# Performance work log

Hardware: AMD Instinct MI355X
Metric: run time of the kernel (lower is better)

The kernel has to match this reference:

```python
import jax, jax.numpy as jnp
import numpy as np

VOCAB = 256
D = 512
L = 2
FFN = 2048
H = 8
HD = D // H  # head dim = random-feature dim m for favor+
B = 2
T = 2048


def setup_inputs() -> dict:
    key = jax.random.key(0)
    ks = jax.random.split(key, 16)
    rng = np.random.default_rng(0)

    def lin(k, fan_in, shape):
        return jax.random.normal(k, shape, jnp.float32) / np.sqrt(fan_in)

    tokens = jax.random.randint(ks[0], (B, T), 0, VOCAB)
    emb = jax.random.normal(ks[1], (VOCAB, D // 2), jnp.float32)
    Wq = lin(ks[2], D, (L, D, D)); bq = 0.01 * jax.random.normal(ks[3], (L, D), jnp.float32)
    Wk = lin(ks[4], D, (L, D, D)); bk = 0.01 * jax.random.normal(ks[5], (L, D), jnp.float32)
    Wv = lin(ks[6], D, (L, D, D)); bv = 0.01 * jax.random.normal(ks[7], (L, D), jnp.float32)
    WU = lin(ks[8], D, (L, D, FFN)); bU = 0.01 * jax.random.normal(ks[9], (L, FFN), jnp.float32)
    WV = lin(ks[10], FFN, (L, FFN, D)); bV = 0.01 * jax.random.normal(ks[11], (L, D), jnp.float32)
    Wout = lin(ks[12], D, (D, VOCAB)); bout = 0.01 * jax.random.normal(ks[13], (VOCAB,), jnp.float32)
    ln1_g = jnp.ones((L, D), jnp.float32) + 0.02 * jax.random.normal(ks[14], (L, D), jnp.float32)
    ln2_g = jnp.ones((L, D), jnp.float32) + 0.02 * jax.random.normal(ks[15], (L, D), jnp.float32)
    ln1_b = jnp.zeros((L, D), jnp.float32)
    ln2_b = jnp.zeros((L, D), jnp.float32)
    # orthogonal random features per (layer, head), scaled by sqrt(head_dim)
    rfs_np = np.stack([
        np.stack([np.linalg.qr(rng.standard_normal((HD, HD)))[0] * np.sqrt(HD) for _ in range(H)])
        for _ in range(L)
    ]).astype(np.float32)
    rfs = jnp.asarray(rfs_np)
    return dict(tokens=tokens, emb=emb, Wq=Wq, bq=bq, Wk=Wk, bk=bk, Wv=Wv, bv=bv,
                rfs=rfs, ln1_g=ln1_g, ln1_b=ln1_b, ln2_g=ln2_g, ln2_b=ln2_b,
                WU=WU, bU=bU, WV=WV, bV=bV, Wout=Wout, bout=bout)


def _layernorm(x, g, b, eps=1e-5):
    mu = jnp.mean(x, -1, keepdims=True)
    var = jnp.mean((x - mu) ** 2, -1, keepdims=True)
    return (x - mu) * jax.lax.rsqrt(var + eps) * g + b


def _favor_feat(x, rfs):
    # x: [B,T,H,d]; rfs: [H,d,m]
    xp = x * (HD ** -0.25)
    return jnp.exp(jnp.einsum('bthd,hdm->bthm', xp, rfs)
                   - 0.5 * jnp.sum(xp ** 2, -1, keepdims=True))


def _attention(x, Wq, bq, Wk, bk, Wv, bv, rfs):
    Bx, Tx, Dm = x.shape
    q = (x @ Wq + bq).reshape(Bx, Tx, H, HD)
    k = (x @ Wk + bk).reshape(Bx, Tx, H, HD)
    v = (x @ Wv + bv).reshape(Bx, Tx, H, HD)
    qf = _favor_feat(q, rfs)  # [B,T,H,m]
    kf = _favor_feat(k, rfs)
    # causal prefix-sum (num_ps / den_ps with zero init sums)
    kv_cum = jnp.cumsum(jnp.einsum('bthm,bthd->bthmd', kf, v), axis=1)
    num = jnp.einsum('bthm,bthmd->bthd', qf, kv_cum)
    den = jnp.einsum('bthm,bthm->bth', qf, jnp.cumsum(kf, axis=1))
    return (num / (den[..., None] + 1e-16)).reshape(Bx, Tx, Dm)


def _pos_embs(x):
    # x: [B,T,D//2]; concat fixed sinusoidal embeddings of size D//2
    Bx, Tx, half = x.shape
    positions = jnp.arange(Tx, dtype=x.dtype)
    freqs = jnp.exp(jnp.arange(0, half, 2, dtype=x.dtype) * (-np.log(10000.0) / half))
    args = positions[:, None] * freqs[None, :]  # [T, half//2]
    sin = jnp.broadcast_to(jnp.sin(args)[None], (Bx, Tx, args.shape[1]))
    cos = jnp.broadcast_to(jnp.cos(args)[None], (Bx, Tx, args.shape[1]))
    return jnp.concatenate([x, sin, cos], -1)


def reference(tokens, emb, Wq, bq, Wk, bk, Wv, bv, rfs,
              ln1_g, ln1_b, ln2_g, ln2_b, WU, bU, WV, bV, Wout, bout):
    x = emb[tokens]            # [B,T,D//2]
    x = _pos_embs(x)           # [B,T,D]
    for i in range(L):
        skip = x
        a = _attention(x, Wq[i], bq[i], Wk[i], bk[i], Wv[i], bv[i], rfs[i])
        a = _layernorm(a, ln1_g[i], ln1_b[i])  # on_gptln=True: LN after attention
        x = skip + a
        skip = x
        h = jax.nn.gelu(x @ WU[i] + bU[i], approximate=False)
        h = h @ WV[i] + bV[i]
        h = _layernorm(h, ln2_g[i], ln2_b[i])  # on_gptln=True: LN after FFN
        x = skip + h
    return x @ Wout + bout     # [B,T,VOCAB]
```

## Files before the change

kernel.cpp:

```cpp
#include <hip/hip_runtime.h>
#include <hip/hip_bf16.h>
#include <math.h>

#define B_  2
#define T_  2048
#define D_  512
#define H_  8
#define HD_ 64
#define FFN_ 2048
#define VOCAB_ 256
#define BT_ (B_*T_)
#define NC_ 32
#define CENT_ 4160

typedef __attribute__((ext_vector_type(8))) short short8;
typedef __attribute__((ext_vector_type(4))) float float4v;
typedef __hip_bfloat16 bf16;

__device__ __forceinline__ void load16_lds(const void* g, void* l) {
  __builtin_amdgcn_global_load_lds(
      (const __attribute__((address_space(1))) unsigned int*)g,
      (__attribute__((address_space(3))) unsigned int*)l,
      16, 0, 0);
}

__global__ __launch_bounds__(512) void embed_pos_kernel(
    const int* __restrict__ tokens, const float* __restrict__ emb,
    float* __restrict__ x, bf16* __restrict__ xb)
{
  int bt = blockIdx.x;
  int t  = bt & (T_ - 1);
  int j  = threadIdx.x;
  float val;
  if (j < 256) {
    int tok = tokens[bt];
    val = emb[tok * 256 + j];
  } else {
    int jj = (j - 256) & 127;
    float f = expf(-(float)(2 * jj) * (9.210340371976184f / 256.0f));
    float arg = (float)t * f;
    val = (j < 384) ? sinf(arg) : cosf(arg);
  }
  size_t off = (size_t)bt * D_ + j;
  x[off]  = val;
  xb[off] = __float2bfloat16(val);
}

__global__ __launch_bounds__(256) void prep_all_kernel(
    const float* __restrict__ Wv, const float* __restrict__ WU,
    const float* __restrict__ WVp, const float* __restrict__ Wout,
    bf16* __restrict__ WvT, bf16* __restrict__ WUT,
    bf16* __restrict__ WVT, bf16* __restrict__ WoutT,
    const float* __restrict__ bq, const float* __restrict__ bk,
    const float* __restrict__ rfs, float* __restrict__ bqf,
    float* __restrict__ bkf)
{
  __shared__ float t[32][33];
  int id = blockIdx.x;
  if (id >= 4736) {
    int z = id - 4736;
    int l = z >> 1, side = z & 1;
    const float* b = (side ? bk : bq) + l * D_;
    float* bo = (side ? bkf : bqf) + l * D_;
    for (int n = threadIdx.x; n < D_; n += 256) {
      int h = n >> 6, j = n & 63;
      const float* R = rfs + ((size_t)l * H_ + h) * 4096;
      float acc = 0.f;
      for (int d = 0; d < 64; ++d) acc += b[h * 64 + d] * R[d * 64 + j];
      bo[n] = acc * 0.35355339059327373f;
    }
    return;
  }
  const float* W; bf16* Wt; int K, N, tx, ty;
  if (id < 512) {
    int l = id >> 8, tt = id & 255;
    W = Wv + (size_t)l * D_ * D_;  Wt = WvT + (size_t)l * D_ * D_;
    K = D_; N = D_; tx = tt & 15; ty = tt >> 4;
  } else if (id < 2560) {
    int tt = id - 512; int l = tt >> 10; tt &= 1023;
    W = WU + (size_t)l * D_ * FFN_;  Wt = WUT + (size_t)l * D_ * FFN_;
    K = D_; N = FFN_; tx = tt & 63; ty = tt >> 6;
  } else if (id < 4608) {
    int tt = id - 2560; int l = tt >> 10; tt &= 1023;
    W = WVp + (size_t)l * FFN_ * D_;  Wt = WVT + (size_t)l * FFN_ * D_;
    K = FFN_; N = D_; tx = tt & 15; ty = tt >> 4;
  } else {
    int tt = id - 4608;
    W = Wout;  Wt = WoutT;
    K = D_; N = VOCAB_; tx = tt & 7; ty = tt >> 3;
  }
  int n0 = tx * 32, k0 = ty * 32;
  int lx = threadIdx.x & 31, ly = threadIdx.x >> 5;
#pragma unroll
  for (int r = 0; r < 4; ++r)
    t[ly + 8 * r][lx] = W[(size_t)(k0 + ly + 8 * r) * N + n0 + lx];
  __syncthreads();
#pragma unroll
  for (int r = 0; r < 4; ++r)
    Wt[(size_t)(n0 + ly + 8 * r) * K + k0 + lx] = __float2bfloat16(t[lx][ly + 8 * r]);
}

__global__ __launch_bounds__(256) void rf_fold_w_kernel(
    const float* __restrict__ Wq, const float* __restrict__ Wk,
    const float* __restrict__ rfs, bf16* __restrict__ WqT, bf16* __restrict__ WkT)
{
  int h = blockIdx.x, kq = blockIdx.y, z = blockIdx.z;
  int l = z >> 1, side = z & 1;
  const float* W = (side ? Wk : Wq) + (size_t)l * D_ * D_;
  bf16* WT = (side ? WkT : WqT) + (size_t)l * D_ * D_;
  const float* Rg = rfs + ((size_t)l * H_ + h) * 4096;
  __shared__ float Rl[64][65];
  __shared__ float Ws[128][65];
  int tid = threadIdx.x;
  for (int i = tid; i < 1024; i += 256) {
    float4 v4 = ((const float4*)Rg)[i];
    int d = i >> 4, j0 = (i & 15) * 4;
    Rl[d][j0] = v4.x; Rl[d][j0+1] = v4.y; Rl[d][j0+2] = v4.z; Rl[d][j0+3] = v4.w;
  }
  for (int i = tid; i < 2048; i += 256) {
    int r = i >> 4, c0 = (i & 15) * 4;
    float4 v4 = *(const float4*)&W[(size_t)(kq * 128 + r) * D_ + h * 64 + c0];
    Ws[r][c0] = v4.x; Ws[r][c0+1] = v4.y; Ws[r][c0+2] = v4.z; Ws[r][c0+3] = v4.w;
  }
  __syncthreads();
  int lane = tid & 63, w = tid >> 6;
  for (int kh = 0; kh < 2; ++kh) {
    int kk = kh * 64 + lane;
#pragma unroll 1
    for (int jj = 0; jj < 16; ++jj) {
      int j = w * 16 + jj;
      float acc = 0.f;
#pragma unroll 16
      for (int d = 0; d < 64; ++d) acc += Ws[kk][d] * Rl[d][j];
      WT[(size_t)(h * 64 + j) * D_ + kq * 128 + kk] =
          __float2bfloat16(acc * 0.35355339059327373f);
    }
  }
}

__device__ __forceinline__ void mfma_core(
    const bf16* __restrict__ A, const bf16* __restrict__ Bt,
    int strideK, int kr, int row0, int col0, float4v acc[4][4])
{
  __shared__ short Al[128 * 32];
  __shared__ short Bl[128 * 32];
  int tid = threadIdx.x;
  int lane = tid & 63, w = tid >> 6;
  int wm = (w >> 1) * 64, wn = (w & 1) * 64;
  int quad = lane >> 4, l16 = lane & 15;

  int r0 = 32 * w + (lane >> 2);
  int ks = (lane & 3) * 8;
  const short* gA0 = (const short*)A + (size_t)(row0 + r0) * strideK + ks;
  const short* gA1 = gA0 + (size_t)16 * strideK;
  const short* gB0 = (const short*)Bt + (size_t)(col0 + r0) * strideK + ks;
  const short* gB1 = gB0 + (size_t)16 * strideK;
  short* lA0 = Al + (32 * w) * 32;
  short* lA1 = Al + (32 * w + 16) * 32;
  short* lB0 = Bl + (32 * w) * 32;
  short* lB1 = Bl + (32 * w + 16) * 32;

  load16_lds(gA0, lA0);
  load16_lds(gA1, lA1);
  load16_lds(gB0, lB0);
  load16_lds(gB1, lB1);

  for (int kt = 0; kt < kr; ++kt) {
    __syncthreads();
    short8 af[4], bfr[4];
#pragma unroll
    for (int mi = 0; mi < 4; ++mi)
      af[mi] = *(const short8*)&Al[(wm + mi * 16 + l16) * 32 + quad * 8];
#pragma unroll
    for (int ni = 0; ni < 4; ++ni)
      bfr[ni] = *(const short8*)&Bl[(wn + ni * 16 + l16) * 32 + quad * 8];
    __syncthreads();
    if (kt + 1 < kr) {
      int o = (kt + 1) * 32;
      load16_lds(gA0 + o, lA0);
      load16_lds(gA1 + o, lA1);
      load16_lds(gB0 + o, lB0);
      load16_lds(gB1 + o, lB1);
    }
#pragma unroll
    for (int mi = 0; mi < 4; ++mi)
#pragma unroll
      for (int ni = 0; ni < 4; ++ni)
        acc[mi][ni] = __builtin_amdgcn_mfma_f32_16x16x32_bf16(
            af[mi], bfr[ni], acc[mi][ni], 0, 0, 0);
  }
}

__global__ __launch_bounds__(256) void gemm_mfma(
    const bf16* __restrict__ A, const bf16* __restrict__ Bt,
    const float* __restrict__ bias, void* __restrict__ Cout,
    int M, int N, int K, int mode)
{
  int lane = threadIdx.x & 63, w = threadIdx.x >> 6;
  int wm = (w >> 1) * 64, wn = (w & 1) * 64;
  int quad = lane >> 4, l16 = lane & 15;
  int row0 = blockIdx.y * 128, col0 = blockIdx.x * 128;
  float4v acc[4][4] = {};
  mfma_core(A, Bt, K, K >> 5, row0, col0, acc);
#pragma unroll
  for (int mi = 0; mi < 4; ++mi) {
#pragma unroll
    for (int ni = 0; ni < 4; ++ni) {
      int j = col0 + wn + ni * 16 + l16;
      float bj = bias[j];
#pragma unroll
      for (int r = 0; r < 4; ++r) {
        int i = row0 + wm + mi * 16 + quad * 4 + r;
        float v = acc[mi][ni][r] + bj;
        if (mode == 1) {
          v = 0.5f * v * (1.0f + erff(v * 0.7071067811865475f));
          ((bf16*)Cout)[(size_t)i * N + j] = __float2bfloat16(v);
        } else {
          ((float*)Cout)[(size_t)i * N + j] = v;
        }
      }
    }
  }
}

__global__ __launch_bounds__(256) void gemm_qkv(
    const bf16* __restrict__ A, const bf16* __restrict__ wT,
    const float* __restrict__ bqf, const float* __restrict__ bkf,
    const float* __restrict__ bv, float* __restrict__ outb, int l)
{
  int z = blockIdx.z;
  const bf16* Bt = wT + ((size_t)z * 2 + l) * D_ * D_;
  const float* bias = (z == 0 ? bqf : (z == 1 ? bkf : bv)) + l * D_;
  float* Cout = outb + (size_t)z * BT_ * D_;
  int lane = threadIdx.x & 63, w = threadIdx.x >> 6;
  int wm = (w >> 1) * 64, wn = (w & 1) * 64;
  int quad = lane >> 4, l16 = lane & 15;
  int row0 = blockIdx.y * 128, col0 = blockIdx.x * 128;
  float4v acc[4][4] = {};
  mfma_core(A, Bt, D_, D_ >> 5, row0, col0, acc);
  if (z < 2) {
#pragma unroll
    for (int mi = 0; mi < 4; ++mi) {
      float vres[4][4];
      float sq[4] = {0.f, 0.f, 0.f, 0.f};
#pragma unroll
      for (int ni = 0; ni < 4; ++ni) {
        int j = col0 + wn + ni * 16 + l16;
        float bj = bias[j];
#pragma unroll
        for (int r = 0; r < 4; ++r) {
          float v = acc[mi][ni][r] + bj;
          vres[ni][r] = v;
          sq[r] += v * v;
        }
      }
#pragma unroll
      for (int r = 0; r < 4; ++r) {
        float s = sq[r];
        s += __shfl_xor(s, 1, 64);
        s += __shfl_xor(s, 2, 64);
        s += __shfl_xor(s, 4, 64);
        s += __shfl_xor(s, 8, 64);
        sq[r] = s;
      }
#pragma unroll
      for (int ni = 0; ni < 4; ++ni) {
        int j = col0 + wn + ni * 16 + l16;
#pragma unroll
        for (int r = 0; r < 4; ++r) {
          int i = row0 + wm + mi * 16 + quad * 4 + r;
          Cout[(size_t)i * D_ + j] = __expf(vres[ni][r] - sq[r] * (1.0f / 128.0f));
        }
      }
    }
  } else {
#pragma unroll
    for (int mi = 0; mi < 4; ++mi) {
#pragma unroll
      for (int ni = 0; ni < 4; ++ni) {
        int j = col0 + wn + ni * 16 + l16;
        float bj = bias[j];
#pragma unroll
        for (int r = 0; r < 4; ++r) {
          int i = row0 + wm + mi * 16 + quad * 4 + r;
          Cout[(size_t)i * D_ + j] = acc[mi][ni][r] + bj;
        }
      }
    }
  }
}

__global__ __launch_bounds__(256) void gemm_splitk(
    const bf16* __restrict__ A, const bf16* __restrict__ Bt,
    float* __restrict__ P, int M, int N, int K, int KS)
{
  int s = blockIdx.z;
  int lane = threadIdx.x & 63, w = threadIdx.x >> 6;
  int wm = (w >> 1) * 64, wn = (w & 1) * 64;
  int quad = lane >> 4, l16 = lane & 15;
  int row0 = blockIdx.y * 128, col0 = blockIdx.x * 128;
  float4v acc[4][4] = {};
  mfma_core((const bf16*)((const short*)A + s * KS),
            (const bf16*)((const short*)Bt + s * KS),
            K, KS >> 5, row0, col0, acc);
  float* Ps = P + (size_t)s * M * N;
#pragma unroll
  for (int mi = 0; mi < 4; ++mi) {
#pragma unroll
    for (int ni = 0; ni < 4; ++ni) {
      int j = col0 + wn + ni * 16 + l16;
#pragma unroll
      for (int r = 0; r < 4; ++r) {
        int i = row0 + wm + mi * 16 + quad * 4 + r;
        Ps[(size_t)i * N + j] = acc[mi][ni][r];
      }
    }
  }
}

__global__ __launch_bounds__(256) void reduce4_bias_kernel(
    const float* __restrict__ P, const float* __restrict__ bias,
    float* __restrict__ C, int MN, int N)
{
  int idx = (blockIdx.x * 256 + threadIdx.x) * 4;
  float4 s0 = *(const float4*)&P[idx];
  float4 s1 = *(const float4*)&P[idx + MN];
  float4 s2 = *(const float4*)&P[idx + 2 * MN];
  float4 s3 = *(const float4*)&P[idx + 3 * MN];
  float4 b  = *(const float4*)&bias[idx & (N - 1)];
  float4 r;
  r.x = s0.x + s1.x + s2.x + s3.x + b.x;
  r.y = s0.y + s1.y + s2.y + s3.y + b.y;
  r.z = s0.z + s1.z + s2.z + s3.z + b.z;
  r.w = s0.w + s1.w + s2.w + s3.w + b.w;
  *(float4*)&C[idx] = r;
}

__global__ __launch_bounds__(256) void reduce_ln_add_kernel(
    const float* __restrict__ P, const float* __restrict__ bias,
    float* __restrict__ x, bf16* __restrict__ xb,
    const float* __restrict__ g, const float* __restrict__ bta)
{
  const int MN = BT_ * D_;
  int row = blockIdx.x;
  int tid = threadIdx.x;
  size_t base = (size_t)row * D_;
  float v0 = P[base + tid] + P[MN + base + tid] + P[2 * MN + base + tid]
           + P[3 * MN + base + tid] + bias[tid];
  float v1 = P[base + tid + 256] + P[MN + base + tid + 256]
           + P[2 * MN + base + tid + 256] + P[3 * MN + base + tid + 256]
           + bias[tid + 256];
  __shared__ float red[4];
  float w = v0 + v1;
  for (int o = 32; o > 0; o >>= 1) w += __shfl_down(w, o, 64);
  if ((tid & 63) == 0) red[tid >> 6] = w;
  __syncthreads();
  float mu = (red[0] + red[1] + red[2] + red[3]) * (1.f / 512.f);
  float d0 = v0 - mu, d1 = v1 - mu;
  __syncthreads();
  w = d0 * d0 + d1 * d1;
  for (int o = 32; o > 0; o >>= 1) w += __shfl_down(w, o, 64);
  if ((tid & 63) == 0) red[tid >> 6] = w;
  __syncthreads();
  float var = (red[0] + red[1] + red[2] + red[3]) * (1.f / 512.f);
  float rs = rsqrtf(var + 1e-5f);
  float n0 = x[base + tid]       + d0 * rs * g[tid]       + bta[tid];
  float n1 = x[base + tid + 256] + d1 * rs * g[tid + 256] + bta[tid + 256];
  x[base + tid]        = n0;
  x[base + tid + 256]  = n1;
  xb[base + tid]       = __float2bfloat16(n0);
  xb[base + tid + 256] = __float2bfloat16(n1);
}

__global__ __launch_bounds__(256) void chunk_sum_kernel(
    const float* __restrict__ kf, const float* __restrict__ v,
    float* __restrict__ buf)
{
  int bh = blockIdx.x / 31;
  int c  = blockIdx.x % 31;
  int b = bh >> 3, h = bh & 7;
  __shared__ float Ks[64][68], Vs[64][68];
  __shared__ float zpart[4][68];
  int tid = threadIdx.x;
  int d = tid & 63, g = tid >> 6;
  for (int t4 = 0; t4 < 64; t4 += 4) {
    int t = t4 + g;
    size_t off = ((size_t)(b * T_ + c * 64 + t) * D_) + h * 64 + d;
    Ks[t][d] = kf[off];
    Vs[t][d] = v[off];
  }
  __syncthreads();
  float acc[16];
#pragma unroll
  for (int i = 0; i < 16; ++i) acc[i] = 0.f;
  for (int t = 0; t < 64; ++t) {
    float vv = Vs[t][d];
#pragma unroll
    for (int i4 = 0; i4 < 4; ++i4) {
      float4 kv = *(const float4*)&Ks[t][g * 16 + i4 * 4];
      acc[i4*4+0] += kv.x * vv;
      acc[i4*4+1] += kv.y * vv;
      acc[i4*4+2] += kv.z * vv;
      acc[i4*4+3] += kv.w * vv;
    }
  }
  float zp = 0.f;
  for (int t = g * 16; t < g * 16 + 16; ++t) zp += Ks[t][d];
  zpart[g][d] = zp;
  size_t bo = (size_t)(bh * 31 + c) * CENT_;
#pragma unroll
  for (int i = 0; i < 16; ++i) buf[bo + (size_t)(g * 16 + i) * 64 + d] = acc[i];
  __syncthreads();
  if (tid < 64)
    buf[bo + 4096 + tid] = zpart[0][tid] + zpart[1][tid] + zpart[2][tid] + zpart[3][tid];
}

__global__ __launch_bounds__(256) void chunk_prefix_kernel(float* __restrict__ buf)
{
  int bh = blockIdx.x / 17;
  int grp = blockIdx.x % 17;
  int e = grp * 256 + threadIdx.x;
  if (e >= CENT_) return;
  size_t base = (size_t)bh * 31 * CENT_ + e;
  float run = 0.f;
  for (int c = 0; c < 31; ++c) {
    run += buf[base + (size_t)c * CENT_];
    buf[base + (size_t)c * CENT_] = run;
  }
}

__global__ __launch_bounds__(256) void chunk_attn_kernel(
    const float* __restrict__ qf, const float* __restrict__ kf,
    const float* __restrict__ v, const float* __restrict__ buf,
    float* __restrict__ out)
{
  int bh = blockIdx.x >> 5;
  int c  = blockIdx.x & 31;
  int b = bh >> 3, h = bh & 7;
  __shared__ float Qs[64][68], Ks[64][68], Vs[64][68];
  __shared__ float dpart[8][68];
  __shared__ float den[64];
  int tid = threadIdx.x;
  int d = tid & 63, g = tid >> 6;
  for (int t4 = 0; t4 < 64; t4 += 4) {
    int t = t4 + g;
    size_t off = ((size_t)(b * T_ + c * 64 + t) * D_) + h * 64 + d;
    Qs[t][d] = qf[off];
    Ks[t][d] = kf[off];
    Vs[t][d] = v[off];
  }
  __syncthreads();
  {
    int i = d;
    float a[16];
#pragma unroll
    for (int jj = 0; jj < 16; ++jj) a[jj] = 0.f;
    for (int m = 0; m < 64; m += 4) {
      float4 qv = *(const float4*)&Qs[i][m];
#pragma unroll
      for (int jj = 0; jj < 16; ++jj) {
        float4 kv = *(const float4*)&Ks[g * 16 + jj][m];
        a[jj] += qv.x * kv.x + qv.y * kv.y + qv.z * kv.z + qv.w * kv.w;
      }
    }
    __syncthreads();
    float rsum = 0.f;
#pragma unroll
    for (int jj = 0; jj < 16; ++jj) {
      int j = g * 16 + jj;
      a[jj] = (j <= i) ? a[jj] : 0.f;
      rsum += a[jj];
    }
#pragma unroll
    for (int j4 = 0; j4 < 4; ++j4)
      *(float4*)&Ks[i][g * 16 + j4 * 4] =
          make_float4(a[j4*4], a[j4*4+1], a[j4*4+2], a[j4*4+3]);
    dpart[g][i] = rsum;
  }
  const float* S0 = buf + (size_t)(bh * 31 + (c - 1)) * CENT_;
  {
    int i = d;
    float qz = 0.f;
    if (c > 0) {
      const float* z0 = S0 + 4096;
      for (int m = g * 16; m < g * 16 + 16; m += 4) {
        float4 qv = *(const float4*)&Qs[i][m];
        qz += qv.x * z0[m] + qv.y * z0[m+1] + qv.z * z0[m+2] + qv.w * z0[m+3];
      }
    }
    dpart[4 + g][i] = qz;
  }
  __syncthreads();
  if (tid < 64)
    den[tid] = dpart[0][tid] + dpart[1][tid] + dpart[2][tid] + dpart[3][tid]
             + dpart[4][tid] + dpart[5][tid] + dpart[6][tid] + dpart[7][tid];
  float acc[16];
#pragma unroll
  for (int ii = 0; ii < 16; ++ii) acc[ii] = 0.f;
  for (int j = 0; j < 64; j += 4) {
    float va = Vs[j][d], vb2 = Vs[j+1][d], vc = Vs[j+2][d], vd2 = Vs[j+3][d];
#pragma unroll
    for (int ii = 0; ii < 16; ++ii) {
      float4 av = *(const float4*)&Ks[g * 16 + ii][j];
      acc[ii] += av.x * va + av.y * vb2 + av.z * vc + av.w * vd2;
    }
  }
  if (c > 0) {
    for (int m = 0; m < 64; m += 4) {
      float sa = S0[(size_t)m * 64 + d];
      float sb2 = S0[(size_t)(m+1) * 64 + d];
      float sc = S0[(size_t)(m+2) * 64 + d];
      float sd2 = S0[(size_t)(m+3) * 64 + d];
#pragma unroll
      for (int ii = 0; ii < 16; ++ii) {
        float4 qv = *(const float4*)&Qs[g * 16 + ii][m];
        acc[ii] += qv.x * sa + qv.y * sb2 + qv.z * sc + qv.w * sd2;
      }
    }
  }
  __syncthreads();
#pragma unroll
  for (int ii = 0; ii < 16; ++ii) {
    int i = g * 16 + ii;
    size_t off = ((size_t)(b * T_ + c * 64 + i) * D_) + h * 64 + d;
    out[off] = acc[ii] / (den[i] + 1e-16f);
  }
}

__global__ __launch_bounds__(256) void ln_add_kernel(
    float* __restrict__ x, bf16* __restrict__ xb, const float* __restrict__ a,
    const float* __restrict__ g, const float* __restrict__ bta)
{
  int row = blockIdx.x;
  int tid = threadIdx.x;
  const float* ar = a + (size_t)row * D_;
  float v0 = ar[tid], v1 = ar[tid + 256];
  __shared__ float red[4];
  float w = v0 + v1;
  for (int o = 32; o > 0; o >>= 1) w += __shfl_down(w, o, 64);
  if ((tid & 63) == 0) red[tid >> 6] = w;
  __syncthreads();
  float mu = (red[0] + red[1] + red[2] + red[3]) * (1.f / 512.f);
  float d0 = v0 - mu, d1 = v1 - mu;
  __syncthreads();
  w = d0 * d0 + d1 * d1;
  for (int o = 32; o > 0; o >>= 1) w += __shfl_down(w, o, 64);
  if ((tid & 63) == 0) red[tid >> 6] = w;
  __syncthreads();
  float var = (red[0] + red[1] + red[2] + red[3]) * (1.f / 512.f);
  float rs = rsqrtf(var + 1e-5f);
  size_t xoff = (size_t)row * D_;
  float n0 = x[xoff + tid]       + d0 * rs * g[tid]       + bta[tid];
  float n1 = x[xoff + tid + 256] + d1 * rs * g[tid + 256] + bta[tid + 256];
  x[xoff + tid]        = n0;
  x[xoff + tid + 256]  = n1;
  xb[xoff + tid]       = __float2bfloat16(n0);
  xb[xoff + tid + 256] = __float2bfloat16(n1);
}

extern "C" void kernel_launch(void* const* d_in, const int* in_sizes, int n_in,
                              void* d_out, int out_size, void* d_ws, size_t ws_size,
                              hipStream_t stream) {
  const int*   tokens = (const int*)  d_in[0];
  const float* emb    = (const float*)d_in[1];
  const float* Wq     = (const float*)d_in[2];
  const float* bq     = (const float*)d_in[3];
  const float* Wk     = (const float*)d_in[4];
  const float* bk     = (const float*)d_in[5];
  const float* Wv     = (const float*)d_in[6];
  const float* bv     = (const float*)d_in[7];
  const float* rfs    = (const float*)d_in[8];
  const float* ln1g   = (const float*)d_in[9];
  const float* ln1b   = (const float*)d_in[10];
  const float* ln2g   = (const float*)d_in[11];
  const float* ln2b   = (const float*)d_in[12];
  const float* WU     = (const float*)d_in[13];
  const float* bU     = (const float*)d_in[14];
  const float* WV     = (const float*)d_in[15];
  const float* bV     = (const float*)d_in[16];
  const float* Wout   = (const float*)d_in[17];
  const float* bout   = (const float*)d_in[18];
  float* out = (float*)d_out;

  const size_t R = (size_t)BT_ * D_;
  float* ws = (float*)d_ws;
  float* x  = ws + 0 * R;
  float* ab = ws + 1 * R;
  float* qb = ws + 2 * R;
  float* kb = ws + 3 * R;
  float* vb = ws + 4 * R;
  float* sb = ws + 5 * R;
  bf16*  xb = (bf16*)(ws + 6 * R);
  bf16*  hb = (bf16*)qb;
  float* pb = ws + 16 * R;
  bf16* wT    = (bf16*)(ws + 6 * R + R / 2);
  bf16* WqT   = wT;
  bf16* WkT   = WqT + (size_t)2 * D_ * D_;
  bf16* WvT   = WkT + (size_t)2 * D_ * D_;
  bf16* WUT   = WvT + (size_t)2 * D_ * D_;
  bf16* WVT   = WUT + (size_t)2 * D_ * FFN_;
  bf16* WoutT = WVT + (size_t)2 * D_ * FFN_;
  float* bqf  = (float*)(WoutT + (size_t)VOCAB_ * D_);
  float* bkf  = bqf + 2 * D_;

  rf_fold_w_kernel<<<dim3(8, 4, 4), 256, 0, stream>>>(Wq, Wk, rfs, WqT, WkT);
  prep_all_kernel<<<4740, 256, 0, stream>>>(
      Wv, WU, WV, Wout, WvT, WUT, WVT, WoutT, bq, bk, rfs, bqf, bkf);

  embed_pos_kernel<<<BT_, 512, 0, stream>>>(tokens, emb, x, xb);

  for (int l = 0; l < 2; ++l) {
    gemm_qkv<<<dim3(D_/128, BT_/128, 3), 256, 0, stream>>>(
        xb, wT, bqf, bkf, bv, qb, l);

    chunk_sum_kernel<<<16 * 31, 256, 0, stream>>>(kb, vb, sb);
    chunk_prefix_kernel<<<16 * 17, 256, 0, stream>>>(sb);
    chunk_attn_kernel<<<16 * NC_, 256, 0, stream>>>(qb, kb, vb, sb, ab);

    ln_add_kernel<<<BT_, 256, 0, stream>>>(x, xb, ab, ln1g + l*D_, ln1b + l*D_);

    gemm_mfma<<<dim3(FFN_/128, BT_/128), 256, 0, stream>>>(
        xb, WUT + (size_t)l*D_*FFN_, bU + l*FFN_, hb, BT_, FFN_, D_, 1);

    gemm_splitk<<<dim3(D_/128, BT_/128, 4), 256, 0, stream>>>(
        hb, WVT + (size_t)l*FFN_*D_, pb, BT_, D_, FFN_, FFN_/4);
    reduce_ln_add_kernel<<<BT_, 256, 0, stream>>>(
        pb, bV + l*D_, x, xb, ln2g + l*D_, ln2b + l*D_);
  }

  gemm_splitk<<<dim3(VOCAB_/128, BT_/128, 4), 256, 0, stream>>>(
      xb, WoutT, pb, BT_, VOCAB_, D_, D_/4);
  reduce4_bias_kernel<<<(BT_*VOCAB_)/1024, 256, 0, stream>>>(
      pb, bout, out, BT_*VOCAB_, VOCAB_);
}
```

Baseline: 386.5 us.

## Double GEMM K-tile to 64 with XOR-swizzled LDS and batch prefix-scan loads

The shared MFMA core now stages a 64-wide K slice per iteration instead of 32. Its LDS layout uses an XOR swizzle on 16-byte slots to avoid bank conflicts, and each loaded tile feeds two MFMAs. This halves the number of barrier pairs and loop iterations per GEMM, at the cost of twice the LDS and more fragment registers, which could lower occupancy. Separately, the chunk prefix kernel now loads all 31 chunk values up front before the running-sum loop, so the global loads are no longer serialized behind each store.

```diff
diff --git a/kernel.cpp b/kernel.cpp
--- a/kernel.cpp
+++ b/kernel.cpp
@@ -142,52 +142,70 @@
     const bf16* __restrict__ A, const bf16* __restrict__ Bt,
     int strideK, int kr, int row0, int col0, float4v acc[4][4])
 {
-  __shared__ short Al[128 * 32];
-  __shared__ short Bl[128 * 32];
+  __shared__ short Al[128 * 64];
+  __shared__ short Bl[128 * 64];
   int tid = threadIdx.x;
   int lane = tid & 63, w = tid >> 6;
   int wm = (w >> 1) * 64, wn = (w & 1) * 64;
   int quad = lane >> 4, l16 = lane & 15;
 
-  int r0 = 32 * w + (lane >> 2);
-  int ks = (lane & 3) * 8;
-  const short* gA0 = (const short*)A + (size_t)(row0 + r0) * strideK + ks;
-  const short* gA1 = gA0 + (size_t)16 * strideK;
-  const short* gB0 = (const short*)Bt + (size_t)(col0 + r0) * strideK + ks;
-  const short* gB1 = gB0 + (size_t)16 * strideK;
-  short* lA0 = Al + (32 * w) * 32;
-  short* lA1 = Al + (32 * w + 16) * 32;
-  short* lB0 = Bl + (32 * w) * 32;
-  short* lB1 = Bl + (32 * w + 16) * 32;
-
-  load16_lds(gA0, lA0);
-  load16_lds(gA1, lA1);
-  load16_lds(gB0, lB0);
-  load16_lds(gB1, lB1);
+  int lr = lane >> 3;
+  int ks = (((lane & 7) ^ lr)) * 8;
+  const short* gA[4]; const short* gB[4];
+  short* lA[4]; short* lB[4];
+#pragma unroll
+  for (int p = 0; p < 4; ++p) {
+    int r = 32 * w + 8 * p;
+    gA[p] = (const short*)A + (size_t)(row0 + r + lr) * strideK + ks;
+    gB[p] = (const short*)Bt + (size_t)(col0 + r + lr) * strideK + ks;
+    lA[p] = Al + r * 64;
+    lB[p] = Bl + r * 64;
+  }
+#pragma unroll
+  for (int p = 0; p < 4; ++p) {
+    load16_lds(gA[p], lA[p]);
+    load16_lds(gB[p], lB[p]);
+  }
 
   for (int kt = 0; kt < kr; ++kt) {
     __syncthreads();
-    short8 af[4], bfr[4];
-#pragma unroll
-    for (int mi = 0; mi < 4; ++mi)
-      af[mi] = *(const short8*)&Al[(wm + mi * 16 + l16) * 32 + quad * 8];
-#pragma unroll
-    for (int ni = 0; ni < 4; ++ni)
-      bfr[ni] = *(const short8*)&Bl[(wn + ni * 16 + l16) * 32 + quad * 8];
+    short8 af[4][2], bfr[4][2];
+#pragma unroll
+    for (int mi = 0; mi < 4; ++mi) {
+      int R = wm + mi * 16 + l16;
+#pragma unroll
+      for (int s = 0; s < 2; ++s) {
+        int slot = (s * 4 + quad) ^ (R & 7);
+        af[mi][s] = *(const short8*)&Al[R * 64 + slot * 8];
+      }
+    }
+#pragma unroll
+    for (int ni = 0; ni < 4; ++ni) {
+      int R = wn + ni * 16 + l16;
+#pragma unroll
+      for (int s = 0; s < 2; ++s) {
+        int slot = (s * 4 + quad) ^ (R & 7);
+        bfr[ni][s] = *(const short8*)&Bl[R * 64 + slot * 8];
+      }
+    }
     __syncthreads();
     if (kt + 1 < kr) {
-      int o = (kt + 1) * 32;
-      load16_lds(gA0 + o, lA0);
-      load16_lds(gA1 + o, lA1);
-      load16_lds(gB0 + o, lB0);
-      load16_lds(gB1 + o, lB1);
+      int o = (kt + 1) * 64;
+#pragma unroll
+      for (int p = 0; p < 4; ++p) {
+        load16_lds(gA[p] + o, lA[p]);
+        load16_lds(gB[p] + o, lB[p]);
+      }
     }
 #pragma unroll
     for (int mi = 0; mi < 4; ++mi)
 #pragma unroll
-      for (int ni = 0; ni < 4; ++ni)
+      for (int ni = 0; ni < 4; ++ni) {
         acc[mi][ni] = __builtin_amdgcn_mfma_f32_16x16x32_bf16(
-            af[mi], bfr[ni], acc[mi][ni], 0, 0, 0);
+            af[mi][0], bfr[ni][0], acc[mi][ni], 0, 0, 0);
+        acc[mi][ni] = __builtin_amdgcn_mfma_f32_16x16x32_bf16(
+            af[mi][1], bfr[ni][1], acc[mi][ni], 0, 0, 0);
+      }
   }
 }
 
@@ -201,7 +219,7 @@
   int quad = lane >> 4, l16 = lane & 15;
   int row0 = blockIdx.y * 128, col0 = blockIdx.x * 128;
   float4v acc[4][4] = {};
-  mfma_core(A, Bt, K, K >> 5, row0, col0, acc);
+  mfma_core(A, Bt, K, K >> 6, row0, col0, acc);
 #pragma unroll
   for (int mi = 0; mi < 4; ++mi) {
 #pragma unroll
@@ -237,7 +255,7 @@
   int quad = lane >> 4, l16 = lane & 15;
   int row0 = blockIdx.y * 128, col0 = blockIdx.x * 128;
   float4v acc[4][4] = {};
-  mfma_core(A, Bt, D_, D_ >> 5, row0, col0, acc);
+  mfma_core(A, Bt, D_, D_ >> 6, row0, col0, acc);
   if (z < 2) {
 #pragma unroll
     for (int mi = 0; mi < 4; ++mi) {
@@ -302,7 +320,7 @@
   float4v acc[4][4] = {};
   mfma_core((const bf16*)((const short*)A + s * KS),
             (const bf16*)((const short*)Bt + s * KS),
-            K, KS >> 5, row0, col0, acc);
+            K, KS >> 6, row0, col0, acc);
   float* Ps = P + (size_t)s * M * N;
 #pragma unroll
   for (int mi = 0; mi < 4; ++mi) {
@@ -422,9 +440,13 @@
   int e = grp * 256 + threadIdx.x;
   if (e >= CENT_) return;
   size_t base = (size_t)bh * 31 * CENT_ + e;
+  float vals[31];
+#pragma unroll
+  for (int c = 0; c < 31; ++c) vals[c] = buf[base + (size_t)c * CENT_];
   float run = 0.f;
+#pragma unroll
   for (int c = 0; c < 31; ++c) {
-    run += buf[base + (size_t)c * CENT_];
+    run += vals[c];
     buf[base + (size_t)c * CENT_] = run;
   }
 }
```

After: 372.6 us. 1.04x faster.
